# Optimization experiments

Measured on AMD Instinct MI355X. Metric: run time of the kernel, lower is better.

## Reference

```python
import jax, jax.numpy as jnp
import numpy as np

N_WAY = 5
K_SHOT = 5
GAMMA = 20.0    # self.gamma
GAMMA2 = 10.0   # self.gamma2
ALPHA = 0.5     # self.katz_factor
EPS = 1e-16


def setup_inputs() -> dict:
    key = jax.random.key(0)
    k1, k2 = jax.random.split(key)
    feat = jax.random.normal(k1, (2 * N_WAY * K_SHOT, 640, 14, 14), dtype=jnp.float32)
    query_y = jax.random.randint(k2, (N_WAY * K_SHOT,), 0, N_WAY, dtype=jnp.int64)
    return {"feat": feat, "query_y": query_y}


def _predicts(feat):
    n_support = N_WAY * K_SHOT
    query = feat[n_support:]                      # (q, c, h, w)
    # adaptive_max_pool2d(query, w) with h == w is the identity, so the
    # (buggy-but-literal) torch code uses the query tensor as "support".
    support = query
    q, c, h, w = query.shape
    hw = h * w
    # class prototypes: mean over shots -> (n_way, c, hw)
    sup = support.reshape(N_WAY, K_SHOT, c, hw).mean(axis=1)
    qry = query.reshape(q, c, hw)
    # cosine metric: l2-normalize along channel axis
    sup = sup / (EPS + jnp.linalg.norm(sup, axis=1, keepdims=True))
    qry = qry / (EPS + jnp.linalg.norm(qry, axis=1, keepdims=True))
    # S[n, m_q, s, m_s] = <qry[n,:,m_q], sup[s,:,m_s]> ; then fold class dim into M_s
    S = jnp.einsum('qcm,scn->qmsn', qry, sup).reshape(q, hw, N_WAY * hw)
    N, M_q, M_s = S.shape
    # row-stochastic transition matrices (exp/max/sum == softmax of gamma*S)
    T_sq = jax.nn.softmax(GAMMA * S, axis=-1)                              # (N, M_q, M_s)
    T_qs = jax.nn.softmax(GAMMA2 * jnp.swapaxes(S, -1, -2), axis=-1)       # (N, M_s, M_q)
    # bipartite block matrix T = [[0, T_sq^T], [T_qs^T, 0]]
    top = jnp.concatenate([jnp.zeros((N, M_s, M_s), S.dtype),
                           jnp.swapaxes(T_sq, -1, -2)], axis=-1)
    bot = jnp.concatenate([jnp.swapaxes(T_qs, -1, -2),
                           jnp.zeros((N, M_q, M_q), S.dtype)], axis=-1)
    T = jnp.concatenate([top, bot], axis=-2)                               # (N, M_s+M_q, M_s+M_q)
    eye = jnp.eye(M_s + M_q, dtype=S.dtype)
    ones = jnp.ones((N, M_s + M_q, 1), S.dtype)
    # (inv(I - a T) - I) @ 1  ==  solve(I - a T, 1) - 1 (same math, no explicit inverse)
    katz = jnp.linalg.solve(eye[None] - ALPHA * T, ones)[..., 0] - 1.0     # (N, M_s+M_q)
    partial = katz[:, :M_s]
    partial = partial / partial.sum(axis=-1, keepdims=True)
    predicts = partial.reshape(N, N_WAY, -1).sum(axis=-1)                  # (N, n_way)
    return predicts


def reference(feat, query_y):
    return _predicts(feat)
```

## Files before the change

kernel.cpp:

```cpp
#include <hip/hip_runtime.h>
#include <math.h>

#define NQ     25
#define NWAY   5
#define KSHOT  5
#define CC     640
#define HW     196
#define NSL    980
#define NSLP   992
#define RPQ    208
#define BROWS  1024
#define MST    200
#define MRA    208
#define GAMMA  20.0f
#define GAMMA2 10.0f
#define NITER  8

typedef __bf16 bf16;
typedef __attribute__((ext_vector_type(8))) __bf16 bf16x8;
typedef __attribute__((ext_vector_type(4))) float f32x4;

__global__ __launch_bounds__(256) void k_norm(const float* __restrict__ feat,
                                              bf16* __restrict__ qnbt,
                                              bf16* __restrict__ snbt) {
    const int by = blockIdx.y;
    const int lx = threadIdx.x & 15;
    const int cg = threadIdx.x >> 4;
    const int l  = blockIdx.x * 16 + lx;
    const bool act = (l < HW);
    const int c0 = cg * 40;
    __shared__ float pr[16][17];

    float xv[40];
    float ss = 0.f;
    if (by < NQ) {
        const float* f = feat + (size_t)(NQ + by) * CC * HW;
#pragma unroll
        for (int i = 0; i < 40; ++i) {
            float x = act ? f[(c0 + i) * HW + l] : 0.f;
            xv[i] = x; ss += x * x;
        }
    } else {
        const int s = by - NQ;
        const float* f = feat + (size_t)(NQ + s * KSHOT) * CC * HW;
        const size_t img = (size_t)CC * HW;
#pragma unroll
        for (int i = 0; i < 40; ++i) {
            float m = 0.f;
            if (act) {
                const float* p = f + (c0 + i) * HW + l;
                m = 0.2f * (p[0] + p[img] + p[2 * img] + p[3 * img] + p[4 * img]);
            }
            xv[i] = m; ss += m * m;
        }
    }
    pr[cg][lx] = ss;
    __syncthreads();
    if (cg == 0) {
        float a = 0.f;
#pragma unroll
        for (int k = 0; k < 16; ++k) a += pr[k][lx];
        pr[0][lx] = 1.f / (1e-16f + sqrtf(a));
    }
    __syncthreads();
    const float inv = pr[0][lx];
    if (act) {
        bf16* o = (by < NQ) ? (qnbt + ((size_t)by * RPQ + l) * CC)
                            : (snbt + ((size_t)(by - NQ) * HW + l) * CC);
#pragma unroll
        for (int i = 0; i < 40; ++i) o[c0 + i] = (bf16)(xv[i] * inv);
    }
}

#define ASTR2 72
__global__ __launch_bounds__(256) void k_sgemm(const bf16* __restrict__ qnbt,
                                               const bf16* __restrict__ snbt,
                                               float* __restrict__ S) {
    const int q  = blockIdx.z;
    const int m0 = blockIdx.y * 80;
    const int n0 = blockIdx.x * 128;
    __shared__ bf16 As[128 * ASTR2];
    __shared__ bf16 Bs[128 * ASTR2];
    const int t = threadIdx.x;
    const int lane = t & 63, w = t >> 6;
    const int wr = w >> 1, wc = w & 1;
    const int lo = lane & 15, hi = lane >> 4;
    const int sr = t >> 1, sh = (t & 1) * 32;

    const bf16* Aq = qnbt + (size_t)q * RPQ * CC;
    f32x4 acc[4][4] = {};

    for (int k0 = 0; k0 < CC; k0 += 64) {
        bf16x8 a0 = *reinterpret_cast<const bf16x8*>(&Aq[(size_t)(m0 + sr) * CC + k0 + sh]);
        bf16x8 a1 = *reinterpret_cast<const bf16x8*>(&Aq[(size_t)(m0 + sr) * CC + k0 + sh + 8]);
        bf16x8 a2 = *reinterpret_cast<const bf16x8*>(&Aq[(size_t)(m0 + sr) * CC + k0 + sh + 16]);
        bf16x8 a3 = *reinterpret_cast<const bf16x8*>(&Aq[(size_t)(m0 + sr) * CC + k0 + sh + 24]);
        bf16x8 b0 = *reinterpret_cast<const bf16x8*>(&snbt[(size_t)(n0 + sr) * CC + k0 + sh]);
        bf16x8 b1 = *reinterpret_cast<const bf16x8*>(&snbt[(size_t)(n0 + sr) * CC + k0 + sh + 8]);
        bf16x8 b2 = *reinterpret_cast<const bf16x8*>(&snbt[(size_t)(n0 + sr) * CC + k0 + sh + 16]);
        bf16x8 b3 = *reinterpret_cast<const bf16x8*>(&snbt[(size_t)(n0 + sr) * CC + k0 + sh + 24]);
        __syncthreads();
        *reinterpret_cast<bf16x8*>(&As[sr * ASTR2 + sh])      = a0;
        *reinterpret_cast<bf16x8*>(&As[sr * ASTR2 + sh + 8])  = a1;
        *reinterpret_cast<bf16x8*>(&As[sr * ASTR2 + sh + 16]) = a2;
        *reinterpret_cast<bf16x8*>(&As[sr * ASTR2 + sh + 24]) = a3;
        *reinterpret_cast<bf16x8*>(&Bs[sr * ASTR2 + sh])      = b0;
        *reinterpret_cast<bf16x8*>(&Bs[sr * ASTR2 + sh + 8])  = b1;
        *reinterpret_cast<bf16x8*>(&Bs[sr * ASTR2 + sh + 16]) = b2;
        *reinterpret_cast<bf16x8*>(&Bs[sr * ASTR2 + sh + 24]) = b3;
        __syncthreads();
#pragma unroll
        for (int kk = 0; kk < 2; ++kk) {
            bf16x8 af[4], bf[4];
#pragma unroll
            for (int mi = 0; mi < 4; ++mi)
                af[mi] = *reinterpret_cast<const bf16x8*>(
                    &As[(wr * 64 + mi * 16 + lo) * ASTR2 + kk * 32 + hi * 8]);
#pragma unroll
            for (int ni = 0; ni < 4; ++ni)
                bf[ni] = *reinterpret_cast<const bf16x8*>(
                    &Bs[(wc * 64 + ni * 16 + lo) * ASTR2 + kk * 32 + hi * 8]);
#pragma unroll
            for (int mi = 0; mi < 4; ++mi)
#pragma unroll
                for (int ni = 0; ni < 4; ++ni)
                    acc[mi][ni] = __builtin_amdgcn_mfma_f32_16x16x32_bf16(af[mi], bf[ni], acc[mi][ni], 0, 0, 0);
        }
    }

    float* Sq = S + (size_t)q * HW * NSL;
#pragma unroll
    for (int mi = 0; mi < 4; ++mi) {
#pragma unroll
        for (int ni = 0; ni < 4; ++ni) {
            const int j = n0 + wc * 64 + ni * 16 + lo;
            if (j >= NSL) continue;
#pragma unroll
            for (int r = 0; r < 4; ++r) {
                const int m = m0 + wr * 64 + mi * 16 + hi * 4 + r;
                if (m < HW) Sq[(size_t)m * NSL + j] = acc[mi][ni][r];
            }
        }
    }
}

#define TSBLK (NQ * HW / 4)
__global__ __launch_bounds__(256) void k_soft(const float* __restrict__ S,
                                              bf16* __restrict__ Ts,
                                              bf16* __restrict__ Tq,
                                              float* __restrict__ R) {
    const int bid = blockIdx.x;
    if (bid < TSBLK) {
        const int lane = threadIdx.x & 63, w = threadIdx.x >> 6;
        const int qm = bid * 4 + w;
        const int q = qm / HW, m = qm - q * HW;
        const float* row = S + (size_t)qm * NSL;
        bf16* orow = Ts + ((size_t)q * RPQ + m) * NSLP;
        float x[16];
        float mx = -1e30f;
#pragma unroll
        for (int p = 0; p < 16; ++p) {
            int j = lane + p * 64;
            x[p] = (j < NSL) ? row[j] : -1e30f;
            mx = fmaxf(mx, x[p]);
        }
        for (int d = 32; d; d >>= 1) mx = fmaxf(mx, __shfl_xor(mx, d));
        float sum = 0.f;
#pragma unroll
        for (int p = 0; p < 16; ++p) {
            x[p] = expf(GAMMA * (x[p] - mx));
            sum += x[p];
        }
        for (int d = 32; d; d >>= 1) sum += __shfl_xor(sum, d);
        const float inv = 1.f / sum;
        float racc[NWAY];
#pragma unroll
        for (int s = 0; s < NWAY; ++s) racc[s] = 0.f;
#pragma unroll
        for (int p = 0; p < 16; ++p) {
            int j = lane + p * 64;
            if (j < NSL) {
                float val = x[p] * inv;
                orow[j] = (bf16)val;
                int cls = j / HW;
#pragma unroll
                for (int s = 0; s < NWAY; ++s) racc[s] += (cls == s) ? val : 0.f;
            } else if (j < NSLP) {
                orow[j] = (bf16)0.f;
            }
        }
#pragma unroll
        for (int s = 0; s < NWAY; ++s)
            for (int d = 32; d; d >>= 1) racc[s] += __shfl_xor(racc[s], d);
        if (lane == 0) {
#pragma unroll
            for (int s = 0; s < NWAY; ++s)
                R[((size_t)q * NWAY + s) * HW + m] = racc[s];
        }
    } else {
        const int idx2 = bid - TSBLK;
        const int q  = idx2 >> 4;
        const int bx = idx2 & 15;
        const int tx = threadIdx.x & 63;
        const int tg = threadIdx.x >> 6;
        const int j  = bx * 64 + tx;
        const int m0 = tg * 49;
        const float* base = S + (size_t)q * HW * NSL;
        bf16* ob = Tq + (size_t)q * RPQ * NSLP;
        __shared__ float rmax[4][64], rsum[4][64];
        float xv[49];
        float mx = -1e30f;
        if (j < NSL) {
#pragma unroll
            for (int i = 0; i < 49; ++i) {
                xv[i] = base[(m0 + i) * NSL + j];
                mx = fmaxf(mx, xv[i]);
            }
        }
        rmax[tg][tx] = mx;
        __syncthreads();
        mx = fmaxf(fmaxf(rmax[0][tx], rmax[1][tx]), fmaxf(rmax[2][tx], rmax[3][tx]));
        float sum = 0.f;
        if (j < NSL) {
#pragma unroll
            for (int i = 0; i < 49; ++i) {
                xv[i] = expf(GAMMA2 * (xv[i] - mx));
                sum += xv[i];
            }
        }
        rsum[tg][tx] = sum;
        __syncthreads();
        const float inv = 1.f / (rsum[0][tx] + rsum[1][tx] + rsum[2][tx] + rsum[3][tx]);
        if (j < NSL) {
#pragma unroll
            for (int i = 0; i < 49; ++i) ob[(size_t)(m0 + i) * NSLP + j] = (bf16)(xv[i] * inv);
        } else if (j < NSLP) {
#pragma unroll
            for (int i = 0; i < 49; ++i) ob[(size_t)(m0 + i) * NSLP + j] = (bf16)0.f;
        }
    }
}

__global__ __launch_bounds__(64) void k_mgemm(const bf16* __restrict__ Tq,
                                              const bf16* __restrict__ Ts,
                                              bf16* __restrict__ Mb,
                                              float* __restrict__ rhs) {
    const int q  = blockIdx.z;
    const int it = blockIdx.y;
    const int jt = blockIdx.x;
    const int l  = threadIdx.x;
    const int lo = l & 15, hi = l >> 4;
    const bool dorhs = (jt == 0);
    const bf16* Ap[4];
    const bf16* Bp[4];
#pragma unroll
    for (int mi = 0; mi < 4; ++mi)
        Ap[mi] = Tq + ((size_t)q * RPQ + it * 64 + mi * 16 + lo) * NSLP + hi * 8;
#pragma unroll
    for (int ni = 0; ni < 4; ++ni)
        Bp[ni] = Ts + ((size_t)q * RPQ + jt * 64 + ni * 16 + lo) * NSLP + hi * 8;

    f32x4 acc[4][4] = {};
    float rsum[4] = {0.f, 0.f, 0.f, 0.f};
#pragma unroll 2
    for (int k0 = 0; k0 < NSLP; k0 += 32) {
        bf16x8 a[4], b[4];
#pragma unroll
        for (int mi = 0; mi < 4; ++mi) a[mi] = *reinterpret_cast<const bf16x8*>(Ap[mi] + k0);
#pragma unroll
        for (int ni = 0; ni < 4; ++ni) b[ni] = *reinterpret_cast<const bf16x8*>(Bp[ni] + k0);
        if (dorhs) {
#pragma unroll
            for (int mi = 0; mi < 4; ++mi)
#pragma unroll
                for (int e = 0; e < 8; ++e) rsum[mi] += (float)a[mi][e];
        }
#pragma unroll
        for (int mi = 0; mi < 4; ++mi)
#pragma unroll
            for (int ni = 0; ni < 4; ++ni)
                acc[mi][ni] = __builtin_amdgcn_mfma_f32_16x16x32_bf16(a[mi], b[ni], acc[mi][ni], 0, 0, 0);
    }

    if (dorhs) {
#pragma unroll
        for (int mi = 0; mi < 4; ++mi) {
            float v = rsum[mi];
            v += __shfl_xor(v, 16);
            v += __shfl_xor(v, 32);
            const int i = it * 64 + mi * 16 + lo;
            if (hi == 0 && i < HW) rhs[q * HW + i] = 1.f + 0.5f * v;
        }
    }

    bf16* Mq = Mb + (size_t)q * MRA * MST;
#pragma unroll
    for (int mi = 0; mi < 4; ++mi) {
#pragma unroll
        for (int ni = 0; ni < 4; ++ni) {
            const int j = jt * 64 + ni * 16 + lo;
            if (j >= MST) continue;
#pragma unroll
            for (int r = 0; r < 4; ++r) {
                const int i = it * 64 + mi * 16 + hi * 4 + r;
                if (i >= MRA) continue;
                Mq[(size_t)i * MST + j] =
                    (i < HW && j < HW) ? (bf16)(0.25f * acc[mi][ni][r]) : (bf16)0.f;
            }
        }
    }
}

__global__ __launch_bounds__(1024) void k_solve2(const bf16* __restrict__ Mb,
                                                 const float* __restrict__ rhs,
                                                 const float* __restrict__ R,
                                                 float* __restrict__ out) {
    const int q = blockIdx.x;
    __shared__ __align__(16) bf16 Ms[HW * MST];
    __shared__ __align__(16) float va[MST], vb[MST];
    __shared__ float part[4][256];
    __shared__ float rhsl[HW];
    __shared__ float cls[NWAY];
    const int t = threadIdx.x, lane = t & 63, w = t >> 6;

    const bf16x8* gm = reinterpret_cast<const bf16x8*>(Mb + (size_t)q * MRA * MST);
    bf16x8* lm = reinterpret_cast<bf16x8*>(Ms);
    for (int i = t; i < HW * (MST / 8); i += 1024) lm[i] = gm[i];

    if (t < MST) {
        float r = (t < HW) ? rhs[q * HW + t] : 0.f;
        if (t < HW) rhsl[t] = r;
        va[t] = r; vb[t] = 0.f;
    }
    __syncthreads();

    const int r = t & 255, qd = t >> 8;
    const int cstart = (qd == 0) ? 0 : 7 + 6 * (qd - 1);
    const int ccnt   = (qd == 0) ? 7 : 6;
    for (int it = 0; it < NITER; ++it) {
        const float* src = (it & 1) ? vb : va;
        float* dst = (it & 1) ? va : vb;
        float a = 0.f;
        if (r < HW) {
            const bf16x8* mrow = reinterpret_cast<const bf16x8*>(&Ms[r * MST]);
            for (int c = cstart; c < cstart + ccnt; ++c) {
                bf16x8 mv = mrow[c];
                const float* sp = &src[c * 8];
#pragma unroll
                for (int e = 0; e < 8; ++e) a += (float)mv[e] * sp[e];
            }
        }
        part[qd][r] = a;
        __syncthreads();
        if (qd == 0 && r < HW)
            dst[r] = rhsl[r] + (part[0][r] + part[1][r] + part[2][r] + part[3][r]);
        __syncthreads();
    }

    if (w < NWAY) {
        const float* Rs = R + ((size_t)q * NWAY + w) * HW;
        float a = 0.f;
        for (int m = lane; m < HW; m += 64) a += va[m] * Rs[m];
        for (int d = 32; d; d >>= 1) a += __shfl_xor(a, d);
        if (lane == 0) cls[w] = a;
    }
    __syncthreads();
    if (t == 0) {
        float tot = cls[0] + cls[1] + cls[2] + cls[3] + cls[4];
        float invt = 1.f / tot;
        for (int s = 0; s < NWAY; ++s) out[q * NWAY + s] = cls[s] * invt;
    }
}

extern "C" void kernel_launch(void* const* d_in, const int* in_sizes, int n_in,
                              void* d_out, int out_size, void* d_ws, size_t ws_size,
                              hipStream_t stream) {
    const float* feat = (const float*)d_in[0];
    float* out = (float*)d_out;
    char* w = (char*)d_ws;

    float* S    = (float*)w;  w += sizeof(float) * (size_t)NQ * HW * NSL;
    bf16*  Ts   = (bf16*)w;   w += sizeof(bf16)  * (size_t)NQ * RPQ * NSLP;
    bf16*  Tq   = (bf16*)w;   w += sizeof(bf16)  * (size_t)NQ * RPQ * NSLP;
    bf16*  qnbt = (bf16*)w;   w += sizeof(bf16)  * (size_t)NQ * RPQ * CC;
    bf16*  snbt = (bf16*)w;   w += sizeof(bf16)  * (size_t)BROWS * CC;
    float* R    = (float*)w;  w += sizeof(float) * (size_t)NQ * NWAY * HW;
    float* rhs  = (float*)w;  w += sizeof(float) * (size_t)NQ * HW;
    bf16* Mb = (bf16*)S;

    k_norm  <<<dim3(13, NQ + NWAY), 256, 0, stream>>>(feat, qnbt, snbt);
    k_sgemm <<<dim3(8, 2, NQ), 256, 0, stream>>>(qnbt, snbt, S);
    k_soft  <<<TSBLK + NQ * 16, 256, 0, stream>>>(S, Ts, Tq, R);
    k_mgemm <<<dim3(4, 4, NQ), 64, 0, stream>>>(Tq, Ts, Mb, rhs);
    k_solve2<<<NQ, 1024, 0, stream>>>(Mb, rhs, R, out);
}
```

Baseline: 103.3 us.

## Store similarity matrix in fp16 and retile transition GEMM with LDS staging

Result: slower. 111.0 us (+7.5%).

```diff
diff --git a/kernel.cpp b/kernel.cpp
--- a/kernel.cpp
+++ b/kernel.cpp
@@ -17,6 +17,7 @@
 #define NITER  8
 
 typedef __bf16 bf16;
+typedef _Float16 f16;
 typedef __attribute__((ext_vector_type(8))) __bf16 bf16x8;
 typedef __attribute__((ext_vector_type(4))) float f32x4;
 
@@ -75,7 +76,7 @@
 #define ASTR2 72
 __global__ __launch_bounds__(256) void k_sgemm(const bf16* __restrict__ qnbt,
                                                const bf16* __restrict__ snbt,
-                                               float* __restrict__ S) {
+                                               f16* __restrict__ S) {
     const int q  = blockIdx.z;
     const int m0 = blockIdx.y * 80;
     const int n0 = blockIdx.x * 128;
@@ -128,7 +129,7 @@
         }
     }
 
-    float* Sq = S + (size_t)q * HW * NSL;
+    f16* Sq = S + (size_t)q * HW * NSL;
 #pragma unroll
     for (int mi = 0; mi < 4; ++mi) {
 #pragma unroll
@@ -138,14 +139,14 @@
 #pragma unroll
             for (int r = 0; r < 4; ++r) {
                 const int m = m0 + wr * 64 + mi * 16 + hi * 4 + r;
-                if (m < HW) Sq[(size_t)m * NSL + j] = acc[mi][ni][r];
+                if (m < HW) Sq[(size_t)m * NSL + j] = (f16)acc[mi][ni][r];
             }
         }
     }
 }
 
 #define TSBLK (NQ * HW / 4)
-__global__ __launch_bounds__(256) void k_soft(const float* __restrict__ S,
+__global__ __launch_bounds__(256) void k_soft(const f16* __restrict__ S,
                                               bf16* __restrict__ Ts,
                                               bf16* __restrict__ Tq,
                                               float* __restrict__ R) {
@@ -154,14 +155,14 @@
         const int lane = threadIdx.x & 63, w = threadIdx.x >> 6;
         const int qm = bid * 4 + w;
         const int q = qm / HW, m = qm - q * HW;
-        const float* row = S + (size_t)qm * NSL;
+        const f16* row = S + (size_t)qm * NSL;
         bf16* orow = Ts + ((size_t)q * RPQ + m) * NSLP;
         float x[16];
         float mx = -1e30f;
 #pragma unroll
         for (int p = 0; p < 16; ++p) {
             int j = lane + p * 64;
-            x[p] = (j < NSL) ? row[j] : -1e30f;
+            x[p] = (j < NSL) ? (float)row[j] : -1e30f;
             mx = fmaxf(mx, x[p]);
         }
         for (int d = 32; d; d >>= 1) mx = fmaxf(mx, __shfl_xor(mx, d));
@@ -205,7 +206,7 @@
         const int tg = threadIdx.x >> 6;
         const int j  = bx * 64 + tx;
         const int m0 = tg * 49;
-        const float* base = S + (size_t)q * HW * NSL;
+        const f16* base = S + (size_t)q * HW * NSL;
         bf16* ob = Tq + (size_t)q * RPQ * NSLP;
         __shared__ float rmax[4][64], rsum[4][64];
         float xv[49];
@@ -213,7 +214,7 @@
         if (j < NSL) {
 #pragma unroll
             for (int i = 0; i < 49; ++i) {
-                xv[i] = base[(m0 + i) * NSL + j];
+                xv[i] = (float)base[(m0 + i) * NSL + j];
                 mx = fmaxf(mx, xv[i]);
             }
         }
@@ -241,56 +242,61 @@
     }
 }
 
-__global__ __launch_bounds__(64) void k_mgemm(const bf16* __restrict__ Tq,
-                                              const bf16* __restrict__ Ts,
-                                              bf16* __restrict__ Mb,
-                                              float* __restrict__ rhs) {
+#define MSTR 40
+__global__ __launch_bounds__(256) void k_mgemm(const bf16* __restrict__ Tq,
+                                               const bf16* __restrict__ Ts,
+                                               bf16* __restrict__ Mb,
+                                               float* __restrict__ rhs) {
     const int q  = blockIdx.z;
-    const int it = blockIdx.y;
-    const int jt = blockIdx.x;
-    const int l  = threadIdx.x;
-    const int lo = l & 15, hi = l >> 4;
-    const bool dorhs = (jt == 0);
-    const bf16* Ap[4];
-    const bf16* Bp[4];
-#pragma unroll
-    for (int mi = 0; mi < 4; ++mi)
-        Ap[mi] = Tq + ((size_t)q * RPQ + it * 64 + mi * 16 + lo) * NSLP + hi * 8;
-#pragma unroll
-    for (int ni = 0; ni < 4; ++ni)
-        Bp[ni] = Ts + ((size_t)q * RPQ + jt * 64 + ni * 16 + lo) * NSLP + hi * 8;
-
+    const int m0 = blockIdx.y * 68;
+    const int n0 = blockIdx.x * 68;
+    __shared__ bf16 As[128 * MSTR];
+    __shared__ bf16 Bs[128 * MSTR];
+    const int t = threadIdx.x;
+    const int lane = t & 63, w = t >> 6;
+    const int wr = w >> 1, wc = w & 1;
+    const int lo = lane & 15, hi = lane >> 4;
+    const int sr = t >> 1, sh = (t & 1) * 16;
+    const bool dorhs = (blockIdx.x == 0);
+
+    const bf16* Aq = Tq + (size_t)q * RPQ * NSLP;
+    const bf16* Bq = Ts + (size_t)q * RPQ * NSLP;
     f32x4 acc[4][4] = {};
-    float rsum[4] = {0.f, 0.f, 0.f, 0.f};
-#pragma unroll 2
+    float rsum = 0.f;
+
     for (int k0 = 0; k0 < NSLP; k0 += 32) {
-        bf16x8 a[4], b[4];
-#pragma unroll
-        for (int mi = 0; mi < 4; ++mi) a[mi] = *reinterpret_cast<const bf16x8*>(Ap[mi] + k0);
-#pragma unroll
-        for (int ni = 0; ni < 4; ++ni) b[ni] = *reinterpret_cast<const bf16x8*>(Bp[ni] + k0);
+        bf16x8 a0 = *reinterpret_cast<const bf16x8*>(&Aq[(size_t)(m0 + sr) * NSLP + k0 + sh]);
+        bf16x8 a1 = *reinterpret_cast<const bf16x8*>(&Aq[(size_t)(m0 + sr) * NSLP + k0 + sh + 8]);
+        bf16x8 b0 = *reinterpret_cast<const bf16x8*>(&Bq[(size_t)(n0 + sr) * NSLP + k0 + sh]);
+        bf16x8 b1 = *reinterpret_cast<const bf16x8*>(&Bq[(size_t)(n0 + sr) * NSLP + k0 + sh + 8]);
         if (dorhs) {
 #pragma unroll
-            for (int mi = 0; mi < 4; ++mi)
-#pragma unroll
-                for (int e = 0; e < 8; ++e) rsum[mi] += (float)a[mi][e];
-        }
+            for (int e = 0; e < 8; ++e) rsum += (float)a0[e] + (float)a1[e];
+        }
+        __syncthreads();
+        *reinterpret_cast<bf16x8*>(&As[sr * MSTR + sh])     = a0;
+        *reinterpret_cast<bf16x8*>(&As[sr * MSTR + sh + 8]) = a1;
+        *reinterpret_cast<bf16x8*>(&Bs[sr * MSTR + sh])     = b0;
+        *reinterpret_cast<bf16x8*>(&Bs[sr * MSTR + sh + 8]) = b1;
+        __syncthreads();
+        bf16x8 af[4], bfr[4];
 #pragma unroll
         for (int mi = 0; mi < 4; ++mi)
+            af[mi] = *reinterpret_cast<const bf16x8*>(&As[(wr * 64 + mi * 16 + lo) * MSTR + hi * 8]);
+#pragma unroll
+        for (int ni = 0; ni < 4; ++ni)
+            bfr[ni] = *reinterpret_cast<const bf16x8*>(&Bs[(wc * 64 + ni * 16 + lo) * MSTR + hi * 8]);
+#pragma unroll
+        for (int mi = 0; mi < 4; ++mi)
 #pragma unroll
             for (int ni = 0; ni < 4; ++ni)
-                acc[mi][ni] = __builtin_amdgcn_mfma_f32_16x16x32_bf16(a[mi], b[ni], acc[mi][ni], 0, 0, 0);
+                acc[mi][ni] = __builtin_amdgcn_mfma_f32_16x16x32_bf16(af[mi], bfr[ni], acc[mi][ni], 0, 0, 0);
     }
 
     if (dorhs) {
-#pragma unroll
-        for (int mi = 0; mi < 4; ++mi) {
-            float v = rsum[mi];
-            v += __shfl_xor(v, 16);
-            v += __shfl_xor(v, 32);
-            const int i = it * 64 + mi * 16 + lo;
-            if (hi == 0 && i < HW) rhs[q * HW + i] = 1.f + 0.5f * v;
-        }
+        rsum += __shfl_xor(rsum, 1);
+        const int i = m0 + sr;
+        if ((t & 1) == 0 && i < HW) rhs[q * HW + i] = 1.f + 0.5f * rsum;
     }
 
     bf16* Mq = Mb + (size_t)q * MRA * MST;
@@ -298,14 +304,11 @@
     for (int mi = 0; mi < 4; ++mi) {
 #pragma unroll
         for (int ni = 0; ni < 4; ++ni) {
-            const int j = jt * 64 + ni * 16 + lo;
-            if (j >= MST) continue;
+            const int j = n0 + wc * 64 + ni * 16 + lo;
 #pragma unroll
             for (int r = 0; r < 4; ++r) {
-                const int i = it * 64 + mi * 16 + hi * 4 + r;
-                if (i >= MRA) continue;
-                Mq[(size_t)i * MST + j] =
-                    (i < HW && j < HW) ? (bf16)(0.25f * acc[mi][ni][r]) : (bf16)0.f;
+                const int i = m0 + wr * 64 + mi * 16 + hi * 4 + r;
+                Mq[(size_t)i * MST + j] = (bf16)(0.25f * acc[mi][ni][r]);
             }
         }
     }
@@ -379,7 +382,7 @@
     float* out = (float*)d_out;
     char* w = (char*)d_ws;
 
-    float* S    = (float*)w;  w += sizeof(float) * (size_t)NQ * HW * NSL;
+    f16*   S    = (f16*)w;    w += sizeof(f16)   * (size_t)NQ * HW * NSL;
     bf16*  Ts   = (bf16*)w;   w += sizeof(bf16)  * (size_t)NQ * RPQ * NSLP;
     bf16*  Tq   = (bf16*)w;   w += sizeof(bf16)  * (size_t)NQ * RPQ * NSLP;
     bf16*  qnbt = (bf16*)w;   w += sizeof(bf16)  * (size_t)NQ * RPQ * CC;
@@ -391,6 +394,6 @@
     k_norm  <<<dim3(13, NQ + NWAY), 256, 0, stream>>>(feat, qnbt, snbt);
     k_sgemm <<<dim3(8, 2, NQ), 256, 0, stream>>>(qnbt, snbt, S);
     k_soft  <<<TSBLK + NQ * 16, 256, 0, stream>>>(S, Ts, Tq, R);
-    k_mgemm <<<dim3(4, 4, NQ), 64, 0, stream>>>(Tq, Ts, Mb, rhs);
+    k_mgemm <<<dim3(2, 2, NQ), 256, 0, stream>>>(Tq, Ts, Mb, rhs);
     k_solve2<<<NQ, 1024, 0, stream>>>(Mb, rhs, R, out);
 }
```
